# Performance work log

Hardware: AMD Instinct MI355X
Metric: run time of the kernel (lower is better)

The kernel has to match this reference:

```python
import jax, jax.numpy as jnp
import numpy as np

IN_F, OUT_F = 4096, 16384
B, S = 4, 2048
SCALE = 0.02

def setup_inputs() -> dict:
    key = jax.random.key(0)
    k1, k2 = jax.random.split(key)
    x = jax.random.normal(k1, (B, S, IN_F), dtype=jnp.float32)
    # ternary weights in {-1, 0, +1}
    weight_ternary = jax.random.randint(k2, (OUT_F, IN_F), -1, 2, dtype=jnp.int32)
    weight_scale = jnp.full((1,), SCALE, dtype=jnp.float32)
    return {"x": x, "weight_ternary": weight_ternary, "weight_scale": weight_scale}

def reference(x, weight_ternary, weight_scale):
    # dequantize ternary weight
    w = weight_ternary.astype(jnp.float32) * weight_scale  # [OUT_F, IN_F]
    # per-token int8 activation quant/dequant
    x_scale = jnp.clip(jnp.max(jnp.abs(x), axis=-1, keepdims=True), 1e-5, None)
    x_quant = jnp.round(jnp.clip(x / x_scale * 127.0, -128.0, 127.0))
    x_final = x_quant * x_scale / 127.0
    # linear: x_final @ w.T
    return jnp.einsum('bsi,oi->bso', x_final, w)
```

## Files before the change

### kernel.cpp

```cpp
#include <hip/hip_runtime.h>

#define IN_F 4096
#define OUT_F 16384
#define MTOK 8192

#define BM 256
#define BN 256
#define BK 64
#define NKT (IN_F / BK)

typedef __attribute__((ext_vector_type(4)))  int   i32x4;
typedef __attribute__((ext_vector_type(4)))  float f32x4;

__device__ __forceinline__ void gload_lds16(const void* g, void* l) {
    __builtin_amdgcn_global_load_lds(
        (const __attribute__((address_space(1))) void*)g,
        (__attribute__((address_space(3))) void*)l,
        16, 0, 0);
}

__global__ __launch_bounds__(256) void k_quant(const float* __restrict__ x,
                                               char* __restrict__ xq,
                                               float* __restrict__ xs) {
    const int m = blockIdx.x;
    const int t = threadIdx.x;
    const float* xrow = x + (size_t)m * IN_F;

    f32x4 v[4];
    float mx = 0.f;
#pragma unroll
    for (int i = 0; i < 4; ++i) {
        v[i] = *(const f32x4*)&xrow[(i * 256 + t) * 4];
        mx = fmaxf(mx, fmaxf(fmaxf(fabsf(v[i].x), fabsf(v[i].y)),
                             fmaxf(fabsf(v[i].z), fabsf(v[i].w))));
    }
#pragma unroll
    for (int off = 32; off > 0; off >>= 1)
        mx = fmaxf(mx, __shfl_xor(mx, off));

    __shared__ float wmax[4];
    const int wid = t >> 6;
    if ((t & 63) == 0) wmax[wid] = mx;
    __syncthreads();
    const float scale = fmaxf(fmaxf(fmaxf(wmax[0], wmax[1]),
                                    fmaxf(wmax[2], wmax[3])), 1e-5f);
    const float inv = 127.0f / scale;

    int* xqi = (int*)(xq + (size_t)m * IN_F);
#pragma unroll
    for (int i = 0; i < 4; ++i) {
        int q0 = (int)rintf(fminf(fmaxf(v[i].x * inv, -128.f), 127.f));
        int q1 = (int)rintf(fminf(fmaxf(v[i].y * inv, -128.f), 127.f));
        int q2 = (int)rintf(fminf(fmaxf(v[i].z * inv, -128.f), 127.f));
        int q3 = (int)rintf(fminf(fmaxf(v[i].w * inv, -128.f), 127.f));
        xqi[i * 256 + t] = (q0 & 255) | ((q1 & 255) << 8) |
                           ((q2 & 255) << 16) | (q3 << 24);
    }
    if (t == 0) xs[m] = scale;
}

__global__ __launch_bounds__(256) void k_wconv(const int* __restrict__ wt,
                                               int* __restrict__ w8) {
    const int total4 = OUT_F * IN_F / 4;
    int idx = blockIdx.x * 256 + threadIdx.x;
    const int stride = gridDim.x * 256;
    for (; idx < total4; idx += stride) {
        i32x4 w = *(const i32x4*)&wt[(size_t)idx * 4];
        w8[idx] = (w.x & 255) | ((w.y & 255) << 8) |
                  ((w.z & 255) << 16) | (w.w << 24);
    }
}

__global__ __launch_bounds__(512, 2) void k_gemm(
    const char*  __restrict__ Aq,
    const char*  __restrict__ Bq,
    const float* __restrict__ xs,
    const float* __restrict__ wsp,
    float*       __restrict__ C) {
    __shared__ __align__(16) char lds[98304];

    const int t    = threadIdx.x;
    const int lane = t & 63;
    const int wid  = t >> 6;
    const int wr   = wid >> 2;
    const int wc   = wid & 3;

    const int bid = blockIdx.x;
    const int bn  = (bid & 7) * 8 + ((bid >> 3) & 7);
    const int bm  = bid >> 6;
    const int mBase = bm * BM;
    const int nBase = bn * BN;

    const int r0 = t >> 2;
    const int c0 = (((t & 3) ^ ((t >> 3) & 3)) << 4);

#define STAGE(kt, bx) do {                                                     \
        const size_t ks = (size_t)(kt) * BK;                                   \
        gload_lds16(Aq + (size_t)(mBase + r0) * IN_F + ks + c0,                \
                    lds + (bx) * 16384 + wid * 1024);                          \
        gload_lds16(Aq + (size_t)(mBase + 128 + r0) * IN_F + ks + c0,          \
                    lds + (bx) * 16384 + 8192 + wid * 1024);                   \
        gload_lds16(Bq + (size_t)(nBase + r0) * IN_F + ks + c0,                \
                    lds + 49152 + (bx) * 16384 + wid * 1024);                  \
        gload_lds16(Bq + (size_t)(nBase + 128 + r0) * IN_F + ks + c0,          \
                    lds + 49152 + (bx) * 16384 + 8192 + wid * 1024);           \
    } while (0)

    const int fOff = (lane & 15) * 64 + ((((lane >> 4) ^ (lane >> 1)) & 3) << 4);
    const char* ldsA = lds + wr * 8192;
    const char* ldsB = lds + 49152 + wc * 4096;

#define BAR()   __builtin_amdgcn_s_barrier()
#define VM4()   asm volatile("s_waitcnt vmcnt(4)" ::: "memory")
#define VM0()   asm volatile("s_waitcnt vmcnt(0)" ::: "memory")

    i32x4 acc[8][4];
#pragma unroll
    for (int i = 0; i < 8; ++i)
#pragma unroll
        for (int j = 0; j < 4; ++j)
            acc[i][j] = (i32x4){0, 0, 0, 0};

    STAGE(0, 0);
    STAGE(1, 1);
    VM4();
    BAR();

    int x = 0, x2 = 2;
    for (int kt = 0; kt < NKT; ++kt) {
        const int xo = x * 16384;
        const bool more = (kt + 2 < NKT);

        i32x4 b[4], a[8];
#pragma unroll
        for (int ni = 0; ni < 4; ++ni)
            b[ni] = *(const i32x4*)(ldsB + xo + ni * 1024 + fOff);
#pragma unroll
        for (int mi = 0; mi < 8; ++mi)
            a[mi] = *(const i32x4*)(ldsA + xo + mi * 1024 + fOff);

        if (more) STAGE(kt + 2, x2);

        __builtin_amdgcn_s_setprio(1);
#pragma unroll
        for (int mi = 0; mi < 8; ++mi)
#pragma unroll
            for (int ni = 0; ni < 4; ++ni)
                acc[mi][ni] = __builtin_amdgcn_mfma_i32_16x16x64_i8(
                    a[mi], b[ni], acc[mi][ni], 0, 0, 0);
        __builtin_amdgcn_s_setprio(0);

        if (more) { VM4(); } else { VM0(); }
        BAR();

        x  = (x  == 2) ? 0 : x  + 1;
        x2 = (x2 == 2) ? 0 : x2 + 1;
    }

    const float wsc = wsp[0] * (1.0f / 127.0f);
#pragma unroll
    for (int mi = 0; mi < 8; ++mi) {
        float rs[4];
#pragma unroll
        for (int r = 0; r < 4; ++r)
            rs[r] = xs[mBase + wr * 128 + mi * 16 + (lane >> 4) * 4 + r] * wsc;
#pragma unroll
        for (int ni = 0; ni < 4; ++ni) {
            const int col = nBase + wc * 64 + ni * 16 + (lane & 15);
#pragma unroll
            for (int r = 0; r < 4; ++r) {
                const int row = mBase + wr * 128 + mi * 16 + (lane >> 4) * 4 + r;
                C[(size_t)row * OUT_F + col] = (float)acc[mi][ni][r] * rs[r];
            }
        }
    }
}

extern "C" void kernel_launch(void* const* d_in, const int* in_sizes, int n_in,
                              void* d_out, int out_size, void* d_ws, size_t ws_size,
                              hipStream_t stream) {
    const float* x   = (const float*)d_in[0];
    const int*   wt  = (const int*)d_in[1];
    const float* wsp = (const float*)d_in[2];
    float* out = (float*)d_out;

    char*  w8 = (char*)d_ws;
    char*  xq = (char*)d_ws + (size_t)OUT_F * IN_F;
    float* xs = (float*)((char*)d_ws + (size_t)OUT_F * IN_F
                                     + (size_t)MTOK * IN_F);

    k_wconv<<<8192, 256, 0, stream>>>(wt, (int*)w8);
    k_quant<<<MTOK, 256, 0, stream>>>(x, xq, xs);

    const int grid = (MTOK / BM) * (OUT_F / BN);
    k_gemm<<<grid, 512, 0, stream>>>(xq, w8, xs, wsp, out);
}
```

Measured before the change: 644.0 us.

## Switch GEMM to 32x32x32 int8 MFMA with split A-fragment loading

Replaces the 16x16x64 int8 MFMA tiling with 32x32x32 MFMAs, so each wave holds a 4x2 grid of 32x32 accumulators. The LDS swizzle is changed to match the new fragment access pattern. The A fragments are loaded in two halves, with an extra barrier between them and the global prefetch moved after the first half. The aim is to cut LDS reads per MFMA and overlap fragment loads with compute. The extra barrier adds sync cost, and the new swizzle may cause bank conflicts.

```diff
diff --git a/kernel.cpp b/kernel.cpp
--- a/kernel.cpp
+++ b/kernel.cpp
@@ -10,6 +10,7 @@
 #define NKT (IN_F / BK)
 
 typedef __attribute__((ext_vector_type(4)))  int   i32x4;
+typedef __attribute__((ext_vector_type(16))) int   i32x16;
 typedef __attribute__((ext_vector_type(4)))  float f32x4;
 
 __device__ __forceinline__ void gload_lds16(const void* g, void* l) {
@@ -84,6 +85,7 @@
     const int wid  = t >> 6;
     const int wr   = wid >> 2;
     const int wc   = wid & 3;
+    const int h    = lane >> 5;
 
     const int bid = blockIdx.x;
     const int bn  = (bid & 7) * 8 + ((bid >> 3) & 7);
@@ -92,7 +94,7 @@
     const int nBase = bn * BN;
 
     const int r0 = t >> 2;
-    const int c0 = (((t & 3) ^ ((t >> 3) & 3)) << 4);
+    const int c0 = ((((t & 3) ^ ((t >> 3) & 3)) ^ ((t >> 5) & 3)) << 4);
 
 #define STAGE(kt, bx) do {                                                     \
         const size_t ks = (size_t)(kt) * BK;                                   \
@@ -106,20 +108,36 @@
                     lds + 49152 + (bx) * 16384 + 8192 + wid * 1024);           \
     } while (0)
 
-    const int fOff = (lane & 15) * 64 + ((((lane >> 4) ^ (lane >> 1)) & 3) << 4);
+    const int vx = ((lane >> 1) ^ (lane >> 3)) & 3;
+    int fOff[2];
+#pragma unroll
+    for (int kk = 0; kk < 2; ++kk)
+        fOff[kk] = (lane & 31) * 64 + (((2 * kk + h) ^ vx) << 4);
     const char* ldsA = lds + wr * 8192;
     const char* ldsB = lds + 49152 + wc * 4096;
+
+#define MFMA8(Af, MIB)                                                         \
+    __builtin_amdgcn_s_setprio(1);                                             \
+    _Pragma("unroll")                                                          \
+    for (int kk = 0; kk < 2; ++kk)                                             \
+        _Pragma("unroll")                                                      \
+        for (int mi = 0; mi < 2; ++mi)                                         \
+            _Pragma("unroll")                                                  \
+            for (int ni = 0; ni < 2; ++ni)                                     \
+                acc[(MIB) + mi][ni] = __builtin_amdgcn_mfma_i32_32x32x32_i8(   \
+                    Af[mi][kk], b[ni][kk], acc[(MIB) + mi][ni], 0, 0, 0);      \
+    __builtin_amdgcn_s_setprio(0);
 
 #define BAR()   __builtin_amdgcn_s_barrier()
 #define VM4()   asm volatile("s_waitcnt vmcnt(4)" ::: "memory")
 #define VM0()   asm volatile("s_waitcnt vmcnt(0)" ::: "memory")
 
-    i32x4 acc[8][4];
-#pragma unroll
-    for (int i = 0; i < 8; ++i)
-#pragma unroll
-        for (int j = 0; j < 4; ++j)
-            acc[i][j] = (i32x4){0, 0, 0, 0};
+    i32x16 acc[4][2];
+#pragma unroll
+    for (int i = 0; i < 4; ++i)
+#pragma unroll
+        for (int j = 0; j < 2; ++j)
+            acc[i][j] = (i32x16)(0);
 
     STAGE(0, 0);
     STAGE(1, 1);
@@ -130,26 +148,28 @@
     for (int kt = 0; kt < NKT; ++kt) {
         const int xo = x * 16384;
         const bool more = (kt + 2 < NKT);
-
-        i32x4 b[4], a[8];
-#pragma unroll
-        for (int ni = 0; ni < 4; ++ni)
-            b[ni] = *(const i32x4*)(ldsB + xo + ni * 1024 + fOff);
-#pragma unroll
-        for (int mi = 0; mi < 8; ++mi)
-            a[mi] = *(const i32x4*)(ldsA + xo + mi * 1024 + fOff);
-
+        i32x4 aLo[2][2], aHi[2][2], b[2][2];
+
+#pragma unroll
+        for (int mi = 0; mi < 2; ++mi)
+#pragma unroll
+            for (int kk = 0; kk < 2; ++kk)
+                aLo[mi][kk] = *(const i32x4*)(ldsA + xo + mi * 2048 + fOff[kk]);
+#pragma unroll
+        for (int ni = 0; ni < 2; ++ni)
+#pragma unroll
+            for (int kk = 0; kk < 2; ++kk)
+                b[ni][kk] = *(const i32x4*)(ldsB + xo + ni * 2048 + fOff[kk]);
+        MFMA8(aLo, 0);
+        BAR();
+
+#pragma unroll
+        for (int mi = 0; mi < 2; ++mi)
+#pragma unroll
+            for (int kk = 0; kk < 2; ++kk)
+                aHi[mi][kk] = *(const i32x4*)(ldsA + xo + (2 + mi) * 2048 + fOff[kk]);
         if (more) STAGE(kt + 2, x2);
-
-        __builtin_amdgcn_s_setprio(1);
-#pragma unroll
-        for (int mi = 0; mi < 8; ++mi)
-#pragma unroll
-            for (int ni = 0; ni < 4; ++ni)
-                acc[mi][ni] = __builtin_amdgcn_mfma_i32_16x16x64_i8(
-                    a[mi], b[ni], acc[mi][ni], 0, 0, 0);
-        __builtin_amdgcn_s_setprio(0);
-
+        MFMA8(aHi, 2);
         if (more) { VM4(); } else { VM0(); }
         BAR();
 
@@ -159,18 +179,18 @@
 
     const float wsc = wsp[0] * (1.0f / 127.0f);
 #pragma unroll
-    for (int mi = 0; mi < 8; ++mi) {
-        float rs[4];
-#pragma unroll
-        for (int r = 0; r < 4; ++r)
-            rs[r] = xs[mBase + wr * 128 + mi * 16 + (lane >> 4) * 4 + r] * wsc;
-#pragma unroll
-        for (int ni = 0; ni < 4; ++ni) {
-            const int col = nBase + wc * 64 + ni * 16 + (lane & 15);
-#pragma unroll
-            for (int r = 0; r < 4; ++r) {
-                const int row = mBase + wr * 128 + mi * 16 + (lane >> 4) * 4 + r;
-                C[(size_t)row * OUT_F + col] = (float)acc[mi][ni][r] * rs[r];
+    for (int mi = 0; mi < 4; ++mi) {
+#pragma unroll
+        for (int rq = 0; rq < 4; ++rq) {
+            const int rowB = mBase + wr * 128 + mi * 32 + rq * 8 + h * 4;
+            const f32x4 s4 = *(const f32x4*)&xs[rowB];
+#pragma unroll
+            for (int ni = 0; ni < 2; ++ni) {
+                const int col = nBase + wc * 64 + ni * 32 + (lane & 31);
+#pragma unroll
+                for (int r = 0; r < 4; ++r)
+                    C[(size_t)(rowB + r) * OUT_F + col] =
+                        (float)acc[mi][ni][rq * 4 + r] * (s4[r] * wsc);
             }
         }
     }
```

After: 691.3 us. 1.07x slower.

## Halve M tile, double-buffer LDS fragment reads in registers, remap block order

Applied to the files above, without the earlier changes.

Shrinks the GEMM block tile from 256x256 to 128x256, halving per-warp accumulators and the A LDS footprint to 72KB. The main loop now preloads the next k-step's A/B fragments from LDS into a second register set while the current MFMAs run, unrolled by two to alternate buffers. Block-to-tile mapping is changed so consecutive blocks walk along M for a fixed N group, improving B reuse in cache. The smaller tile lowers arithmetic intensity per block and doubles the block count, and waiting on vmcnt(0) each step removes some of the global-load overlap.

```diff
diff --git a/kernel.cpp b/kernel.cpp
--- a/kernel.cpp
+++ b/kernel.cpp
@@ -4,7 +4,7 @@
 #define OUT_F 16384
 #define MTOK 8192
 
-#define BM 256
+#define BM 128
 #define BN 256
 #define BK 64
 #define NKT (IN_F / BK)
@@ -77,7 +77,7 @@
     const float* __restrict__ xs,
     const float* __restrict__ wsp,
     float*       __restrict__ C) {
-    __shared__ __align__(16) char lds[98304];
+    __shared__ __align__(16) char lds[73728];
 
     const int t    = threadIdx.x;
     const int lane = t & 63;
@@ -86,8 +86,9 @@
     const int wc   = wid & 3;
 
     const int bid = blockIdx.x;
-    const int bn  = (bid & 7) * 8 + ((bid >> 3) & 7);
-    const int bm  = bid >> 6;
+    const int idx = bid >> 3;
+    const int bn  = (bid & 7) * 8 + (idx >> 6);
+    const int bm  = idx & 63;
     const int mBase = bm * BM;
     const int nBase = bn * BN;
 
@@ -97,79 +98,85 @@
 #define STAGE(kt, bx) do {                                                     \
         const size_t ks = (size_t)(kt) * BK;                                   \
         gload_lds16(Aq + (size_t)(mBase + r0) * IN_F + ks + c0,                \
-                    lds + (bx) * 16384 + wid * 1024);                          \
-        gload_lds16(Aq + (size_t)(mBase + 128 + r0) * IN_F + ks + c0,          \
-                    lds + (bx) * 16384 + 8192 + wid * 1024);                   \
+                    lds + (bx) * 8192 + wid * 1024);                           \
         gload_lds16(Bq + (size_t)(nBase + r0) * IN_F + ks + c0,                \
-                    lds + 49152 + (bx) * 16384 + wid * 1024);                  \
+                    lds + 24576 + (bx) * 16384 + wid * 1024);                  \
         gload_lds16(Bq + (size_t)(nBase + 128 + r0) * IN_F + ks + c0,          \
-                    lds + 49152 + (bx) * 16384 + 8192 + wid * 1024);           \
+                    lds + 24576 + (bx) * 16384 + 8192 + wid * 1024);           \
     } while (0)
 
     const int fOff = (lane & 15) * 64 + ((((lane >> 4) ^ (lane >> 1)) & 3) << 4);
-    const char* ldsA = lds + wr * 8192;
-    const char* ldsB = lds + 49152 + wc * 4096;
+    const char* ldsA = lds + wr * 4096;
+    const char* ldsB = lds + 24576 + wc * 4096;
+
+#define RDF(av, bv, xA, xB) do {                                               \
+        _Pragma("unroll")                                                      \
+        for (int mi = 0; mi < 4; ++mi)                                         \
+            av[mi] = *(const i32x4*)(ldsA + (xA) + mi * 1024 + fOff);          \
+        _Pragma("unroll")                                                      \
+        for (int ni = 0; ni < 4; ++ni)                                         \
+            bv[ni] = *(const i32x4*)(ldsB + (xB) + ni * 1024 + fOff);          \
+    } while (0)
+
+#define MFMA16(av, bv)                                                         \
+    __builtin_amdgcn_s_setprio(1);                                             \
+    _Pragma("unroll")                                                          \
+    for (int mi = 0; mi < 4; ++mi)                                             \
+        _Pragma("unroll")                                                      \
+        for (int ni = 0; ni < 4; ++ni)                                         \
+            acc[mi][ni] = __builtin_amdgcn_mfma_i32_16x16x64_i8(               \
+                av[mi], bv[ni], acc[mi][ni], 0, 0, 0);                         \
+    __builtin_amdgcn_s_setprio(0);
 
 #define BAR()   __builtin_amdgcn_s_barrier()
-#define VM4()   asm volatile("s_waitcnt vmcnt(4)" ::: "memory")
 #define VM0()   asm volatile("s_waitcnt vmcnt(0)" ::: "memory")
 
-    i32x4 acc[8][4];
-#pragma unroll
-    for (int i = 0; i < 8; ++i)
+    i32x4 acc[4][4];
+#pragma unroll
+    for (int i = 0; i < 4; ++i)
 #pragma unroll
         for (int j = 0; j < 4; ++j)
             acc[i][j] = (i32x4){0, 0, 0, 0};
 
+    i32x4 a0[4], b0[4], a1[4], b1[4];
+
     STAGE(0, 0);
     STAGE(1, 1);
-    VM4();
+    VM0();
     BAR();
-
-    int x = 0, x2 = 2;
-    for (int kt = 0; kt < NKT; ++kt) {
-        const int xo = x * 16384;
-        const bool more = (kt + 2 < NKT);
-
-        i32x4 b[4], a[8];
-#pragma unroll
-        for (int ni = 0; ni < 4; ++ni)
-            b[ni] = *(const i32x4*)(ldsB + xo + ni * 1024 + fOff);
-#pragma unroll
-        for (int mi = 0; mi < 8; ++mi)
-            a[mi] = *(const i32x4*)(ldsA + xo + mi * 1024 + fOff);
-
-        if (more) STAGE(kt + 2, x2);
-
-        __builtin_amdgcn_s_setprio(1);
-#pragma unroll
-        for (int mi = 0; mi < 8; ++mi)
-#pragma unroll
-            for (int ni = 0; ni < 4; ++ni)
-                acc[mi][ni] = __builtin_amdgcn_mfma_i32_16x16x64_i8(
-                    a[mi], b[ni], acc[mi][ni], 0, 0, 0);
-        __builtin_amdgcn_s_setprio(0);
-
-        if (more) { VM4(); } else { VM0(); }
-        BAR();
-
-        x  = (x  == 2) ? 0 : x  + 1;
-        x2 = (x2 == 2) ? 0 : x2 + 1;
+    RDF(a0, b0, 0, 0);
+
+    int x1A = 8192, x1B = 16384, x2 = 2;
+
+#define BODY(kt, AC, BC, AN, BN_) do {                                         \
+        if ((kt) + 2 < NKT) STAGE((kt) + 2, x2);                               \
+        if ((kt) + 1 < NKT) RDF(AN, BN_, x1A, x1B);                            \
+        MFMA16(AC, BC);                                                        \
+        if ((kt) + 2 < NKT) { VM0(); BAR(); }                                  \
+        x1A = (x1A == 16384) ? 0 : x1A + 8192;                                 \
+        x1B = (x1B == 32768) ? 0 : x1B + 16384;                                \
+        x2  = (x2 == 2) ? 0 : x2 + 1;                                          \
+    } while (0)
+
+    for (int it = 0; it < NKT / 2; ++it) {
+        const int k0 = 2 * it;
+        BODY(k0,     a0, b0, a1, b1);
+        BODY(k0 + 1, a1, b1, a0, b0);
     }
 
     const float wsc = wsp[0] * (1.0f / 127.0f);
 #pragma unroll
-    for (int mi = 0; mi < 8; ++mi) {
+    for (int mi = 0; mi < 4; ++mi) {
         float rs[4];
 #pragma unroll
         for (int r = 0; r < 4; ++r)
-            rs[r] = xs[mBase + wr * 128 + mi * 16 + (lane >> 4) * 4 + r] * wsc;
+            rs[r] = xs[mBase + wr * 64 + mi * 16 + (lane >> 4) * 4 + r] * wsc;
 #pragma unroll
         for (int ni = 0; ni < 4; ++ni) {
             const int col = nBase + wc * 64 + ni * 16 + (lane & 15);
 #pragma unroll
             for (int r = 0; r < 4; ++r) {
-                const int row = mBase + wr * 128 + mi * 16 + (lane >> 4) * 4 + r;
+                const int row = mBase + wr * 64 + mi * 16 + (lane >> 4) * 4 + r;
                 C[(size_t)row * OUT_F + col] = (float)acc[mi][ni][r] * rs[r];
             }
         }
```

Result: slower. 1.028 ms (+59.7%).
